# Performance work log

Hardware: AMD Instinct MI355X
Metric: run time of the kernel (lower is better)

The kernel has to match this reference:

```python
import jax, jax.numpy as jnp
import numpy as np

B, L, D, H = 8, 1024, 1024, 16
DH = D // H  # 64


def setup_inputs() -> dict:
    key = jax.random.key(0)
    ks = jax.random.split(key, 6)
    x = jax.random.normal(ks[0], (B, L, D), dtype=jnp.float32)
    mask = jax.random.randint(ks[1], (1, L, L), 0, 2).astype(jnp.float32)
    # params initialized ~ normal(std=0.1) as in the module's _initialize
    Wk = jax.random.normal(ks[2], (D, D), dtype=jnp.float32) * 0.1
    Wv = jax.random.normal(ks[3], (D, D), dtype=jnp.float32) * 0.1
    Wq = jax.random.normal(ks[4], (D, D), dtype=jnp.float32) * 0.1
    Wo = jax.random.normal(ks[5], (D, D), dtype=jnp.float32) * 0.1
    return {"x": x, "mask": mask, "Wk": Wk, "Wv": Wv, "Wq": Wq, "Wo": Wo}


def reference(x, mask, Wk, Wv, Wq, Wo):
    # torch Linear: y = x @ W.T
    k = jnp.einsum('bld,ed->ble', x, Wk).reshape(B, L, H, DH)
    v = jnp.einsum('bld,ed->ble', x, Wv).reshape(B, L, H, DH)
    q = jnp.einsum('bld,ed->ble', x, Wq).reshape(B, L, H, DH)
    # explicit score matrix [B, H, L, L]
    scores = jnp.einsum('blhe,bmhe->bhlm', q, k)
    m = mask[:, None]  # (1, 1, L, L) broadcasts over batch and heads
    scores = scores * m - 1e9 * (1.0 - m)
    scale = np.float32(1.0 / np.sqrt(DH))
    weights = jax.nn.softmax(scores * scale, axis=-1)
    out = jnp.einsum('bhlm,bmhe->blhe', weights, v).reshape(B, L, D)
    out = jnp.einsum('bld,ed->ble', out, Wo)  # output_linear (n_heads > 1)
    return out
```

## Files before the change

### kernel.cpp

```cpp
#include <hip/hip_runtime.h>

#define B_  8
#define L_  1024
#define D_  1024
#define H_  16
#define DH_ 64

typedef unsigned short u16;
typedef __attribute__((ext_vector_type(8))) short short8;
typedef __attribute__((ext_vector_type(8))) _Float16 half8;
typedef __attribute__((ext_vector_type(4))) float floatx4;
typedef __attribute__((ext_vector_type(16))) float floatx16;

static __device__ __forceinline__ u16 f2bf(float f) {
  union { float f; unsigned u; } cv; cv.f = f;
  unsigned u = cv.u;
  return (u16)((u + 0x7fffu + ((u >> 16) & 1u)) >> 16);
}
static __device__ __forceinline__ u16 f2h(float f) {
  union { _Float16 h; u16 u; } cv; cv.h = (_Float16)f; return cv.u;
}
static __device__ __forceinline__ unsigned pack_bf2(float a, float b) {
  union { float f; unsigned u; } ua, ub; ua.f = a; ub.f = b;
  return __builtin_amdgcn_perm(ub.u + 0x8000u, ua.u + 0x8000u, 0x07060302u);
}

#if __has_builtin(__builtin_amdgcn_exp2f)
#define EXP2(x) __builtin_amdgcn_exp2f(x)
#else
#define EXP2(x) __expf((x) * 0.6931471805599453f)
#endif

__global__ void cast_all(const float* __restrict__ x,  const float* __restrict__ wq,
                         const float* __restrict__ wk, const float* __restrict__ wv,
                         const float* __restrict__ wo, const float* __restrict__ mask,
                         u16* __restrict__ xf,  u16* __restrict__ wqf,
                         u16* __restrict__ wkf, u16* __restrict__ wvf,
                         u16* __restrict__ wof, float* __restrict__ biasP) {
  int blk = blockIdx.x;
  if (blk >= 12288) {
    int i = (blk - 12288) * 256 + threadIdx.x;
    int e = i & 3, lane = (i >> 2) & 63, rr = (i >> 8) & 3, t = (i >> 10) & 1;
    int c = (i >> 11) & 15, w = (i >> 15) & 3, qt = i >> 17;
    int kk  = e + 8 * rr + 4 * (lane >> 5);
    int row = qt * 128 + w * 32 + (lane & 31);
    int key = c * 64 + t * 32 + kk;
    biasP[i] = (mask[(size_t)row * L_ + key] - 1.0f) * 1.8033688e8f - 34.624681f;
    return;
  }
  const float* src; u16* dst; int off;
  if (blk < 8192)       { src = x;  dst = xf;  off = blk; }
  else if (blk < 9216)  { src = wq; dst = wqf; off = blk - 8192; }
  else if (blk < 10240) { src = wk; dst = wkf; off = blk - 9216; }
  else if (blk < 11264) { src = wv; dst = wvf; off = blk - 10240; }
  else                  { src = wo; dst = wof; off = blk - 11264; }
  int i = off * 1024 + threadIdx.x * 4;
  float4 f = *(const float4*)(src + i);
  ushort4 r;
  r.x = f2h(f.x); r.y = f2h(f.y); r.z = f2h(f.z); r.w = f2h(f.w);
  *(ushort4*)(dst + i) = r;
}

typedef __attribute__((address_space(3))) void  lds_void;
typedef const __attribute__((address_space(1))) void g_void;
static __device__ __forceinline__ void load_lds16(const void* g, void* l) {
  __builtin_amdgcn_global_load_lds((g_void*)g, (lds_void*)l, 16, 0, 0);
}

__global__ __launch_bounds__(512, 2) void gemm_qkv(const u16* __restrict__ A,
                                                   const u16* __restrict__ wq,
                                                   const u16* __restrict__ wk,
                                                   const u16* __restrict__ wv,
                                                   u16* __restrict__ qf,
                                                   u16* __restrict__ kf,
                                                   u16* __restrict__ vb) {
  const int K = D_;
  __shared__ u16 lA4[4 * 8192];
  __shared__ u16 lB4[4 * 8192];

  int flat = blockIdx.y * 12 + blockIdx.x;
  int swz  = (flat & 7) * 48 + (flat >> 3);
  int nb   = swz % 12;
  int mb   = swz / 12;

  const u16* Bw; u16* Cp; float scale; int obf;
  int wsel = nb >> 2;
  if (wsel == 0)      { Bw = wq; Cp = qf; scale = 0.18033688f; obf = 0; }
  else if (wsel == 1) { Bw = wk; Cp = kf; scale = 1.0f;        obf = 0; }
  else                { Bw = wv; Cp = vb; scale = 1.0f;        obf = 1; }
  const int m0g = mb * 256;
  const int n0w = (nb & 3) * 256;

  const int tid  = threadIdx.x;
  const int wid  = tid >> 6;
  const int lane = tid & 63;
  const int m16  = lane & 15;
  const int kg   = lane >> 4;
  const int xorv = m16 & 7;
  const int wm   = wid >> 2;
  const int wn   = wid & 3;

  const int ldaBase = m16 * 64 + (((wm * 4 + kg) ^ xorv) * 8);
  const int ldbBase = ((wn & 1) * 64 + m16) * 64 + ((((wn >> 1) * 4 + kg) ^ xorv) * 8);

  const int cl0 = tid,       rho0 = cl0 >> 3;
  const int c0  = (cl0 & 7) ^ (rho0 & 7);
  const int mr0 = rho0 + ((c0 >> 2) << 7), kb0 = c0 & 3;
  const int cl1 = 512 + tid, rho1 = cl1 >> 3;
  const int c1  = (cl1 & 7) ^ (rho1 & 7);
  const int mr1 = rho1 + ((c1 >> 2) << 7), kb1 = c1 & 3;

  const u16* srcA0 = A  + (size_t)(m0g + mr0) * K + kb0 * 8;
  const u16* srcA1 = A  + (size_t)(m0g + mr1) * K + kb1 * 8;
  const u16* srcB0 = Bw + (size_t)(n0w + mr0) * K + kb0 * 8;
  const u16* srcB1 = Bw + (size_t)(n0w + mr1) * K + kb1 * 8;
  const int dst0 = wid * 512;
  const int dst1 = 4096 + wid * 512;

  floatx4 acc[8][4];
#pragma unroll
  for (int i = 0; i < 8; ++i)
#pragma unroll
    for (int j = 0; j < 4; ++j)
#pragma unroll
      for (int r = 0; r < 4; ++r) acc[i][j][r] = 0.0f;

  load_lds16(srcA0, lA4 + 0 * 8192 + dst0);
  load_lds16(srcB0, lB4 + 0 * 8192 + dst0);
  load_lds16(srcA1, lA4 + 0 * 8192 + dst1);
  load_lds16(srcB1, lB4 + 0 * 8192 + dst1);
  load_lds16(srcA0 + 32, lA4 + 1 * 8192 + dst0);
  load_lds16(srcB0 + 32, lB4 + 1 * 8192 + dst0);
  load_lds16(srcA1 + 32, lA4 + 1 * 8192 + dst1);
  load_lds16(srcB1 + 32, lB4 + 1 * 8192 + dst1);
  asm volatile("s_waitcnt vmcnt(4)" ::: "memory");
  __builtin_amdgcn_s_barrier();

  auto TILE = [&](int t, int buf) {
    const u16* bA = lA4 + buf * 8192;
    const u16* bB = lB4 + buf * 8192;
    const int t2 = t + 2;
    const int kk = t2 * 32;
    half8 af[8], bf[4];
#pragma unroll
    for (int i = 0; i < 4; ++i) af[i] = *(const half8*)&bA[ldaBase + i * 1024];
#pragma unroll
    for (int i = 0; i < 4; ++i) bf[i] = *(const half8*)&bB[ldbBase + i * 1024];
    if (t2 < 32) {
      load_lds16(srcA0 + kk, lA4 + (t2 & 3) * 8192 + dst0);
      load_lds16(srcB0 + kk, lB4 + (t2 & 3) * 8192 + dst0);
    }
    __builtin_amdgcn_s_barrier();
    __builtin_amdgcn_s_setprio(1);
#pragma unroll
    for (int i = 0; i < 4; ++i)
#pragma unroll
      for (int j = 0; j < 4; ++j)
        acc[i][j] = __builtin_amdgcn_mfma_f32_16x16x32_f16(af[i], bf[j], acc[i][j], 0, 0, 0);
    __builtin_amdgcn_s_setprio(0);
    __builtin_amdgcn_s_barrier();
#pragma unroll
    for (int i = 4; i < 8; ++i) af[i] = *(const half8*)&bA[ldaBase + i * 1024];
    if (t2 < 32) {
      load_lds16(srcA1 + kk, lA4 + (t2 & 3) * 8192 + dst1);
      load_lds16(srcB1 + kk, lB4 + (t2 & 3) * 8192 + dst1);
    }
    __builtin_amdgcn_s_barrier();
    __builtin_amdgcn_s_setprio(1);
#pragma unroll
    for (int i = 4; i < 8; ++i)
#pragma unroll
      for (int j = 0; j < 4; ++j)
        acc[i][j] = __builtin_amdgcn_mfma_f32_16x16x32_f16(af[i], bf[j], acc[i][j], 0, 0, 0);
    __builtin_amdgcn_s_setprio(0);
    if (t < 30)       asm volatile("s_waitcnt vmcnt(4)" ::: "memory");
    else if (t == 30) asm volatile("s_waitcnt vmcnt(0)" ::: "memory");
    __builtin_amdgcn_s_barrier();
  };

  for (int tt = 0; tt < 32; tt += 4) {
    TILE(tt + 0, 0);
    TILE(tt + 1, 1);
    TILE(tt + 2, 2);
    TILE(tt + 3, 3);
  }

#pragma unroll
  for (int fm = 0; fm < 8; ++fm)
#pragma unroll
    for (int fn = 0; fn < 4; ++fn)
#pragma unroll
      for (int r = 0; r < 4; ++r) {
        int row = m0g + wm * 128 + fm * 16 + kg * 4 + r;
        int col = (nb & 3) * 256 + wn * 64 + fn * 16 + m16;
        float vv = acc[fm][fn][r] * scale;
        Cp[(size_t)row * D_ + col] = obf ? f2bf(vv) : f2h(vv);
      }
}

__global__ __launch_bounds__(256) void gemm_fin(const u16* __restrict__ A,
                                                const u16* __restrict__ Bw,
                                                float* __restrict__ Cp,
                                                int M, int N, int K) {
  __shared__ u16 lA[2 * 128 * 32];
  __shared__ u16 lB[2 * 128 * 32];
  const int tid  = threadIdx.x;
  const int w    = tid >> 6;
  const int lane = tid & 63;
  const int m    = lane & 15;
  const int kg   = lane >> 4;
  const int m0   = blockIdx.y * 128;
  const int n0   = blockIdx.x * 128;
  const int wm   = (w >> 1) * 64;
  const int wn   = (w & 1) * 64;
  const int rowS = tid >> 2;
  const int part = tid & 3;
  const int csrc8 = ((part ^ ((rowS >> 1) & 3))) * 8;
  const int kgs   = (kg ^ ((m >> 1) & 3)) * 8;

  floatx4 acc[4][4];
#pragma unroll
  for (int i = 0; i < 4; ++i)
#pragma unroll
    for (int j = 0; j < 4; ++j)
#pragma unroll
      for (int r = 0; r < 4; ++r) acc[i][j][r] = 0.0f;

  auto STAGE = [&](int k0, int bufsel) {
#pragma unroll
    for (int rnd = 0; rnd < 2; ++rnd) {
      const u16* ga = A  + (size_t)(m0 + rnd * 64 + rowS) * K + k0 + csrc8;
      const u16* gb = Bw + (size_t)(n0 + rnd * 64 + rowS) * K + k0 + csrc8;
      load_lds16(ga, lA + bufsel * 4096 + rnd * 2048 + w * 512);
      load_lds16(gb, lB + bufsel * 4096 + rnd * 2048 + w * 512);
    }
  };

  STAGE(0, 0);
  STAGE(32, 1);

  for (int k0 = 0; k0 < K; k0 += 32) {
    const int buf = (k0 >> 5) & 1;
    if (k0 + 32 < K) { asm volatile("s_waitcnt vmcnt(4)" ::: "memory"); }
    else             { asm volatile("s_waitcnt vmcnt(0)" ::: "memory"); }
    __builtin_amdgcn_s_barrier();
    __builtin_amdgcn_sched_barrier(0);

    const u16* pA = lA + buf * 4096;
    const u16* pB = lB + buf * 4096;
    half8 af[4], bf[4];
#pragma unroll
    for (int i = 0; i < 4; ++i) af[i] = *(const half8*)&pA[(wm + i * 16 + m) * 32 + kgs];
#pragma unroll
    for (int i = 0; i < 4; ++i) bf[i] = *(const half8*)&pB[(wn + i * 16 + m) * 32 + kgs];
#pragma unroll
    for (int mi = 0; mi < 4; ++mi)
#pragma unroll
      for (int ni = 0; ni < 4; ++ni)
        acc[mi][ni] = __builtin_amdgcn_mfma_f32_16x16x32_f16(af[mi], bf[ni], acc[mi][ni], 0, 0, 0);

    __builtin_amdgcn_sched_barrier(0);
    __builtin_amdgcn_s_barrier();
    if (k0 + 64 < K) STAGE(k0 + 64, buf);
  }

#pragma unroll
  for (int mi = 0; mi < 4; ++mi)
#pragma unroll
    for (int ni = 0; ni < 4; ++ni)
#pragma unroll
      for (int r = 0; r < 4; ++r) {
        int row = m0 + wm + mi * 16 + kg * 4 + r;
        int col = n0 + wn + ni * 16 + m;
        Cp[(size_t)row * N + col] = acc[mi][ni][r];
      }
}

__global__ __launch_bounds__(256) void transpose_v(const u16* __restrict__ v,
                                                   u16* __restrict__ vt) {
  __shared__ u16 lds[64][72];
  const int b  = blockIdx.y >> 4;
  const int h  = blockIdx.y & 15;
  const int l0 = blockIdx.x * 64;
  const int tid = threadIdx.x;
#pragma unroll
  for (int it = 0; it < 2; ++it) {
    int idx = it * 256 + tid;
    int i = idx >> 3, off = (idx & 7) * 8;
    *(short8*)&lds[i][off] =
        *(const short8*)(v + ((size_t)(b * L_ + l0 + i)) * D_ + h * 64 + off);
  }
  __syncthreads();
  const int j  = tid >> 2;
  const int p0 = (tid & 3) * 16;
  __attribute__((aligned(16))) u16 tmp[16];
#pragma unroll
  for (int s = 0; s < 16; ++s) {
    int p = p0 + s;
    int l = (p >> 1) + ((p & 1) << 5);
    tmp[s] = lds[l][j];
  }
  u16* dst = vt + ((size_t)((b * H_ + h) * DH_ + j)) * L_ + l0 + p0;
  *(short8*)(dst)     = *(const short8*)&tmp[0];
  *(short8*)(dst + 8) = *(const short8*)&tmp[8];
}

__global__ __launch_bounds__(256, 4) void attn_kernel(const u16* __restrict__ q,
                                                      const u16* __restrict__ k,
                                                      const u16* __restrict__ vt,
                                                      const float* __restrict__ biasP,
                                                      u16* __restrict__ o) {
  __shared__ u16 lK[64][72];
  __shared__ u16 lVt[64][72];
  __shared__ float lRS[4][32];

  const int bh = blockIdx.x, qt = blockIdx.y;
  const int b = bh >> 4, h = bh & 15;
  const int tid = threadIdx.x;
  const int w = tid >> 6, lane = tid & 63;
  const int c32 = lane & 31, hi = lane >> 5;
  const int qr0 = qt * 128 + w * 32;

  const int srow  = tid >> 3;
  const int skoff = (tid & 7) * 8;

  const size_t qbase = ((size_t)((b * L_ + qr0 + c32) * H_ + h)) * DH_;
  half8 aq[4];
#pragma unroll
  for (int ks = 0; ks < 4; ++ks)
    aq[ks] = *(const half8*)(q + qbase + ks * 16 + hi * 8);

  floatx16 acc0, acc1;
#pragma unroll
  for (int i = 0; i < 16; ++i) { acc0[i] = 0.0f; acc1[i] = 0.0f; }
  float rsum0 = 0.0f, rsum1 = 0.0f;

  const u16* kp = k  + ((size_t)((b * L_ + srow) * H_ + h)) * DH_ + skoff;
  const u16* vp = vt + ((size_t)((b * H_ + h) * DH_ + srow)) * L_ + skoff;

  short8 rk[2], rv[2];
#pragma unroll
  for (int it = 0; it < 2; ++it) {
    rk[it] = *(const short8*)(kp + (size_t)it * 32 * H_ * DH_);
    rv[it] = *(const short8*)(vp + (size_t)it * 32 * L_);
  }

  const float4* bp = (const float4*)(biasP + ((size_t)(qt * 4 + w) * 16) * 2048) + lane;

  for (int c = 0; c < 16; ++c) {
    __syncthreads();
#pragma unroll
    for (int it = 0; it < 2; ++it) {
      *(short8*)&lK[it * 32 + srow][skoff]  = rk[it];
      *(short8*)&lVt[it * 32 + srow][skoff] = rv[it];
    }
    __syncthreads();

    floatx16 s0, s1;
#pragma unroll
    for (int rr = 0; rr < 4; ++rr) {
      float4 b0 = bp[rr * 64];
      float4 b1 = bp[(4 + rr) * 64];
      s0[rr * 4 + 0] = b0.x; s0[rr * 4 + 1] = b0.y; s0[rr * 4 + 2] = b0.z; s0[rr * 4 + 3] = b0.w;
      s1[rr * 4 + 0] = b1.x; s1[rr * 4 + 1] = b1.y; s1[rr * 4 + 2] = b1.z; s1[rr * 4 + 3] = b1.w;
    }
    bp += 512;

    if (c < 15) {
      kp += (size_t)64 * H_ * DH_;
      vp += 64;
#pragma unroll
      for (int it = 0; it < 2; ++it) {
        rk[it] = *(const short8*)(kp + (size_t)it * 32 * H_ * DH_);
        rv[it] = *(const short8*)(vp + (size_t)it * 32 * L_);
      }
    }

#pragma unroll
    for (int ks = 0; ks < 4; ++ks) {
      half8 bk0 = *(const half8*)&lK[c32][ks * 16 + hi * 8];
      half8 bk1 = *(const half8*)&lK[32 + c32][ks * 16 + hi * 8];
      s0 = __builtin_amdgcn_mfma_f32_32x32x16_f16(bk0, aq[ks], s0, 0, 0, 0);
      s1 = __builtin_amdgcn_mfma_f32_32x32x16_f16(bk1, aq[ks], s1, 0, 0, 0);
    }

    union { short8 v[4]; unsigned u[16]; } ap;
#pragma unroll
    for (int reg = 0; reg < 16; ++reg) {
      float p0 = EXP2(s0[reg]);
      float p1 = EXP2(s1[reg]);
      ap.u[reg] = pack_bf2(p0, p1);
      if (reg & 1) rsum1 += p0 + p1; else rsum0 += p0 + p1;
    }

#pragma unroll
    for (int ks = 0; ks < 4; ++ks) {
      short8 bv0 = *(const short8*)&lVt[c32][ks * 16 + hi * 8];
      short8 bv1 = *(const short8*)&lVt[32 + c32][ks * 16 + hi * 8];
      acc0 = __builtin_amdgcn_mfma_f32_32x32x16_bf16(ap.v[ks], bv0, acc0, 0, 0, 0);
      acc1 = __builtin_amdgcn_mfma_f32_32x32x16_bf16(ap.v[ks], bv1, acc1, 0, 0, 0);
    }
  }

  float rsum = rsum0 + rsum1;
  rsum += __shfl_xor(rsum, 32, 64);
  if (hi == 0) lRS[w][c32] = rsum;

#pragma unroll
  for (int reg = 0; reg < 16; ++reg) {
    int rl = (reg & 3) + 8 * (reg >> 2) + 4 * hi;
    float inv = 1.0f / lRS[w][rl];
    int row = qr0 + rl;
    size_t obase = ((size_t)((b * L_ + row) * H_ + h)) * DH_;
    o[obase + c32]      = f2h(acc0[reg] * inv);
    o[obase + 32 + c32] = f2h(acc1[reg] * inv);
  }
}

extern "C" void kernel_launch(void* const* d_in, const int* in_sizes, int n_in,
                              void* d_out, int out_size, void* d_ws, size_t ws_size,
                              hipStream_t stream) {
  const float* x    = (const float*)d_in[0];
  const float* mask = (const float*)d_in[1];
  const float* Wk   = (const float*)d_in[2];
  const float* Wv   = (const float*)d_in[3];
  const float* Wq   = (const float*)d_in[4];
  const float* Wo   = (const float*)d_in[5];

  char* ws = (char*)d_ws;
  u16* xf    = (u16*)(ws);
  u16* aout  = xf;
  u16* kf    = (u16*)(ws + (16ull << 20));
  u16* vtb   = (u16*)(ws + (32ull << 20));
  float* biasP = (float*)(ws + (48ull << 20));
  u16* wqf   = (u16*)(ws + (52ull << 20));
  u16* wkf   = (u16*)(ws + (54ull << 20));
  u16* wvf   = (u16*)(ws + (56ull << 20));
  u16* wof   = (u16*)(ws + (58ull << 20));
  u16* qf = (u16*)d_out;
  u16* vb = qf + (size_t)B_ * L_ * D_;

  cast_all<<<16384, 256, 0, stream>>>(x, Wq, Wk, Wv, Wo, mask,
                                      xf, wqf, wkf, wvf, wof, biasP);

  gemm_qkv<<<dim3(12, 32), 512, 0, stream>>>(xf, wqf, wkf, wvf, qf, kf, vb);

  transpose_v<<<dim3(L_ / 64, B_ * H_), 256, 0, stream>>>(vb, vtb);

  attn_kernel<<<dim3(B_ * H_, L_ / 128), 256, 0, stream>>>(qf, kf, vtb, biasP, aout);

  gemm_fin<<<dim3(D_ / 128, (B_ * L_) / 128), 256, 0, stream>>>(
      aout, wof, (float*)d_out, B_ * L_, D_, D_);
}
```

Measured before the change: 254.0 us.

## Shrink QKV GEMM LDS ring from four stages to double buffering

Replaces the four-deep LDS staging ring in the QKV projection GEMM with a two-buffer scheme. Each tile now issues all four next-tile loads at once and waits for them to fully drain before the closing barrier. The launch-bound occupancy hint rises from 2 to 4 blocks, relying on the halved LDS footprint. The cost is less prefetch distance, so global-load latency may be exposed more often.

```diff
diff --git a/kernel.cpp b/kernel.cpp
--- a/kernel.cpp
+++ b/kernel.cpp
@@ -67,7 +67,7 @@
   __builtin_amdgcn_global_load_lds((g_void*)g, (lds_void*)l, 16, 0, 0);
 }
 
-__global__ __launch_bounds__(512, 2) void gemm_qkv(const u16* __restrict__ A,
+__global__ __launch_bounds__(512, 4) void gemm_qkv(const u16* __restrict__ A,
                                                    const u16* __restrict__ wq,
                                                    const u16* __restrict__ wk,
                                                    const u16* __restrict__ wv,
@@ -75,8 +75,8 @@
                                                    u16* __restrict__ kf,
                                                    u16* __restrict__ vb) {
   const int K = D_;
-  __shared__ u16 lA4[4 * 8192];
-  __shared__ u16 lB4[4 * 8192];
+  __shared__ u16 lA2[2 * 8192];
+  __shared__ u16 lB2[2 * 8192];
 
   int flat = blockIdx.y * 12 + blockIdx.x;
   int swz  = (flat & 7) * 48 + (flat >> 3);
@@ -125,30 +125,28 @@
 #pragma unroll
       for (int r = 0; r < 4; ++r) acc[i][j][r] = 0.0f;
 
-  load_lds16(srcA0, lA4 + 0 * 8192 + dst0);
-  load_lds16(srcB0, lB4 + 0 * 8192 + dst0);
-  load_lds16(srcA1, lA4 + 0 * 8192 + dst1);
-  load_lds16(srcB1, lB4 + 0 * 8192 + dst1);
-  load_lds16(srcA0 + 32, lA4 + 1 * 8192 + dst0);
-  load_lds16(srcB0 + 32, lB4 + 1 * 8192 + dst0);
-  load_lds16(srcA1 + 32, lA4 + 1 * 8192 + dst1);
-  load_lds16(srcB1 + 32, lB4 + 1 * 8192 + dst1);
-  asm volatile("s_waitcnt vmcnt(4)" ::: "memory");
+  load_lds16(srcA0, lA2 + dst0);
+  load_lds16(srcB0, lB2 + dst0);
+  load_lds16(srcA1, lA2 + dst1);
+  load_lds16(srcB1, lB2 + dst1);
+  asm volatile("s_waitcnt vmcnt(0)" ::: "memory");
   __builtin_amdgcn_s_barrier();
 
   auto TILE = [&](int t, int buf) {
-    const u16* bA = lA4 + buf * 8192;
-    const u16* bB = lB4 + buf * 8192;
-    const int t2 = t + 2;
-    const int kk = t2 * 32;
+    const u16* bA = lA2 + buf * 8192;
+    const u16* bB = lB2 + buf * 8192;
+    const int nx = (t + 1) * 32;
+    const int ob = (buf ^ 1) * 8192;
     half8 af[8], bf[4];
 #pragma unroll
     for (int i = 0; i < 4; ++i) af[i] = *(const half8*)&bA[ldaBase + i * 1024];
 #pragma unroll
     for (int i = 0; i < 4; ++i) bf[i] = *(const half8*)&bB[ldbBase + i * 1024];
-    if (t2 < 32) {
-      load_lds16(srcA0 + kk, lA4 + (t2 & 3) * 8192 + dst0);
-      load_lds16(srcB0 + kk, lB4 + (t2 & 3) * 8192 + dst0);
+    if (t + 1 < 32) {
+      load_lds16(srcA0 + nx, lA2 + ob + dst0);
+      load_lds16(srcB0 + nx, lB2 + ob + dst0);
+      load_lds16(srcA1 + nx, lA2 + ob + dst1);
+      load_lds16(srcB1 + nx, lB2 + ob + dst1);
     }
     __builtin_amdgcn_s_barrier();
     __builtin_amdgcn_s_setprio(1);
@@ -161,10 +159,6 @@
     __builtin_amdgcn_s_barrier();
 #pragma unroll
     for (int i = 4; i < 8; ++i) af[i] = *(const half8*)&bA[ldaBase + i * 1024];
-    if (t2 < 32) {
-      load_lds16(srcA1 + kk, lA4 + (t2 & 3) * 8192 + dst1);
-      load_lds16(srcB1 + kk, lB4 + (t2 & 3) * 8192 + dst1);
-    }
     __builtin_amdgcn_s_barrier();
     __builtin_amdgcn_s_setprio(1);
 #pragma unroll
@@ -173,16 +167,13 @@
       for (int j = 0; j < 4; ++j)
         acc[i][j] = __builtin_amdgcn_mfma_f32_16x16x32_f16(af[i], bf[j], acc[i][j], 0, 0, 0);
     __builtin_amdgcn_s_setprio(0);
-    if (t < 30)       asm volatile("s_waitcnt vmcnt(4)" ::: "memory");
-    else if (t == 30) asm volatile("s_waitcnt vmcnt(0)" ::: "memory");
+    if (t + 1 < 32) asm volatile("s_waitcnt vmcnt(0)" ::: "memory");
     __builtin_amdgcn_s_barrier();
   };
 
-  for (int tt = 0; tt < 32; tt += 4) {
+  for (int tt = 0; tt < 32; tt += 2) {
     TILE(tt + 0, 0);
     TILE(tt + 1, 1);
-    TILE(tt + 2, 2);
-    TILE(tt + 3, 3);
   }
 
 #pragma unroll
```

After: 691.4 us. 2.72x slower.
